# Optimization experiments

Hardware: AMD Instinct MI355X
Metric: run time of the kernel (lower is better)

## Reference

```python
import jax, jax.numpy as jnp
import numpy as np

EPS = 1e-10   # eps added inside cumprod, as in _compute_weights
FAR = 1e10    # last delta, as in forward()
NEAR_D, FAR_D = 2.0, 6.0  # typical NeRF near/far bounds for depth sampling

N_RAYS, N_PTS = 65536, 128


def setup_inputs() -> dict:
    key = jax.random.key(0)
    k1, k2, k3 = jax.random.split(key, 3)
    # densities are non-negative (raw sigma output after relu/softplus)
    density = jax.random.uniform(k1, (N_RAYS, N_PTS), dtype=jnp.float32) * 2.0
    feature = jax.random.uniform(k2, (N_RAYS, N_PTS, 3), dtype=jnp.float32)
    # monotonically increasing sample depths along each ray in [NEAR_D, FAR_D]
    depth_values = jnp.sort(
        jax.random.uniform(k3, (N_RAYS, N_PTS), dtype=jnp.float32,
                           minval=NEAR_D, maxval=FAR_D), axis=-1)
    return {"density": density, "feature": feature, "depth_values": depth_values}


def reference(density, feature, depth_values):
    # deltas: diff of sample depths, last delta = 1e10  -> [N, P]
    deltas = jnp.concatenate(
        [depth_values[..., 1:] - depth_values[..., :-1],
         jnp.full_like(depth_values[..., :1], FAR)], axis=-1)
    alpha = 1.0 - jnp.exp(-deltas * density)                      # [N, P]
    # transmittance: cumprod(1-alpha+eps) rolled right with T[...,0]=1
    Tinc = jnp.cumprod(1.0 - alpha + EPS, axis=-1)                # [N, P]
    T = jnp.concatenate([jnp.ones_like(Tinc[..., :1]), Tinc[..., :-1]], axis=-1)
    weights = T * alpha                                           # [N, P]
    # weighted feature (rgb) and depth aggregation over samples
    rgb = jnp.einsum('np,npc->nc', weights, feature)              # [N, 3]
    depth = jnp.einsum('np,npc->nc', weights,
                       jnp.broadcast_to(depth_values[..., None], feature.shape))  # [N, 3]
    return rgb, depth
```

## Files before the change

kernel.cpp:

```cpp
#include <hip/hip_runtime.h>

#define N_PTS 128
#define EPS_F 1e-10f
#define FAR_F 1e10f

template<int CTRL, int ROW_MASK>
__device__ __forceinline__ float dpp_mov(float src, float old) {
    union { float f; int i; } s, o, r;
    s.f = src; o.f = old;
    r.i = __builtin_amdgcn_update_dpp(o.i, s.i, CTRL, ROW_MASK, 0xF, false);
    return r.f;
}

__device__ __forceinline__ float wave64_reduce_add(float x) {
    x += dpp_mov<0x111, 0xF>(x, 0.0f);
    x += dpp_mov<0x112, 0xF>(x, 0.0f);
    x += dpp_mov<0x114, 0xF>(x, 0.0f);
    x += dpp_mov<0x118, 0xF>(x, 0.0f);
    x += dpp_mov<0x142, 0xA>(x, 0.0f);
    x += dpp_mov<0x143, 0xC>(x, 0.0f);
    return x;
}

__global__ __launch_bounds__(256) void volrend_kernel(
        const float* __restrict__ density,
        const float* __restrict__ feature,
        const float* __restrict__ depth,
        float* __restrict__ out, int n_rays) {
    const int lane = threadIdx.x & 63;
    const int ray  = blockIdx.x * 4 + (threadIdx.x >> 6);
    if (ray >= n_rays) return;

    const float2 dns = ((const float2*)(density + (size_t)ray * N_PTS))[lane];
    const float2 z   = ((const float2*)(depth   + (size_t)ray * N_PTS))[lane];
    const float2* fp = (const float2*)(feature + (size_t)ray * (N_PTS * 3));
    const float2 fa = fp[lane * 3 + 0];
    const float2 fb = fp[lane * 3 + 1];
    const float2 fc = fp[lane * 3 + 2];

    float nz     = dpp_mov<0x130, 0xF>(z.x, 0.0f);
    float delta0 = z.y - z.x;
    float delta1 = (lane == 63) ? FAR_F : (nz - z.y);

    float e0 = __expf(-delta0 * dns.x);
    float e1 = __expf(-delta1 * dns.y);
    float alpha0 = 1.0f - e0;
    float alpha1 = 1.0f - e1;
    float f0 = e0 + EPS_F;
    float f1 = e1 + EPS_F;

    float p = f0 * f1;
    p *= dpp_mov<0x111, 0xF>(p, 1.0f);
    p *= dpp_mov<0x112, 0xF>(p, 1.0f);
    p *= dpp_mov<0x114, 0xF>(p, 1.0f);
    p *= dpp_mov<0x118, 0xF>(p, 1.0f);
    p *= dpp_mov<0x142, 0xA>(p, 1.0f);
    p *= dpp_mov<0x143, 0xC>(p, 1.0f);
    float T0 = dpp_mov<0x138, 0xF>(p, 1.0f);

    float w0 = T0 * alpha0;
    float T1 = T0 * f0;
    float w1 = T1 * alpha1;

    float rx = wave64_reduce_add(w0 * fa.x + w1 * fb.y);
    float ry = wave64_reduce_add(w0 * fa.y + w1 * fc.x);
    float rz = wave64_reduce_add(w0 * fb.x + w1 * fc.y);
    float dd = wave64_reduce_add(w0 * z.x  + w1 * z.y);

    if (lane == 63) {
        float* o  = out + (size_t)ray * 3;
        o[0] = rx; o[1] = ry; o[2] = rz;
        float* od = out + (size_t)n_rays * 3 + (size_t)ray * 3;
        od[0] = dd; od[1] = dd; od[2] = dd;
    }
}

extern "C" void kernel_launch(void* const* d_in, const int* in_sizes, int n_in,
                              void* d_out, int out_size, void* d_ws, size_t ws_size,
                              hipStream_t stream) {
    const float* density = (const float*)d_in[0];
    const float* feature = (const float*)d_in[1];
    const float* depth   = (const float*)d_in[2];
    float* out = (float*)d_out;
    const int n_rays = in_sizes[0] / N_PTS;
    const int blocks = (n_rays + 3) / 4;
    volrend_kernel<<<blocks, 256, 0, stream>>>(density, feature, depth, out, n_rays);
}
```

Before: 188.9 us.

## Use persistent grid with half-wave per ray, float4 loads, and register prefetch

Each 64-lane wave now processes two rays, with 32 lanes per ray and four samples per lane loaded as float4. The launch becomes a persistent grid of at most 2048 blocks, each looping over ray groups and prefetching the next group's data into registers while computing the current one. Outputs are staged through double-buffered shared memory so they can be written coalesced by a few threads. The aim is wider memory transactions and hidden load latency. In exchange it adds a block-wide barrier per iteration and higher register pressure, and it assumes n_rays is a multiple of 8.

```diff
diff --git a/kernel.cpp b/kernel.cpp
--- a/kernel.cpp
+++ b/kernel.cpp
@@ -3,6 +3,8 @@
 #define N_PTS 128
 #define EPS_F 1e-10f
 #define FAR_F 1e10f
+#define RAYS_PER_BLOCK 8
+#define MAX_GRID 2048
 
 template<int CTRL, int ROW_MASK>
 __device__ __forceinline__ float dpp_mov(float src, float old) {
@@ -12,13 +14,12 @@
     return r.f;
 }
 
-__device__ __forceinline__ float wave64_reduce_add(float x) {
+__device__ __forceinline__ float half32_reduce_add(float x) {
     x += dpp_mov<0x111, 0xF>(x, 0.0f);
     x += dpp_mov<0x112, 0xF>(x, 0.0f);
     x += dpp_mov<0x114, 0xF>(x, 0.0f);
     x += dpp_mov<0x118, 0xF>(x, 0.0f);
     x += dpp_mov<0x142, 0xA>(x, 0.0f);
-    x += dpp_mov<0x143, 0xC>(x, 0.0f);
     return x;
 }
 
@@ -26,52 +27,95 @@
         const float* __restrict__ density,
         const float* __restrict__ feature,
         const float* __restrict__ depth,
-        float* __restrict__ out, int n_rays) {
+        float* __restrict__ out, int n_rays, int iters) {
     const int lane = threadIdx.x & 63;
-    const int ray  = blockIdx.x * 4 + (threadIdx.x >> 6);
-    if (ray >= n_rays) return;
+    const int sub  = lane & 31;
+    const int h    = lane >> 5;
+    const int wid  = threadIdx.x >> 6;
+    const int stride8 = gridDim.x * RAYS_PER_BLOCK;
 
-    const float2 dns = ((const float2*)(density + (size_t)ray * N_PTS))[lane];
-    const float2 z   = ((const float2*)(depth   + (size_t)ray * N_PTS))[lane];
-    const float2* fp = (const float2*)(feature + (size_t)ray * (N_PTS * 3));
-    const float2 fa = fp[lane * 3 + 0];
-    const float2 fb = fp[lane * 3 + 1];
-    const float2 fc = fp[lane * 3 + 2];
+    __shared__ float sbuf[2][64];
 
-    float nz     = dpp_mov<0x130, 0xF>(z.x, 0.0f);
-    float delta0 = z.y - z.x;
-    float delta1 = (lane == 63) ? FAR_F : (nz - z.y);
+    int base8 = blockIdx.x * RAYS_PER_BLOCK;
 
-    float e0 = __expf(-delta0 * dns.x);
-    float e1 = __expf(-delta1 * dns.y);
-    float alpha0 = 1.0f - e0;
-    float alpha1 = 1.0f - e1;
-    float f0 = e0 + EPS_F;
-    float f1 = e1 + EPS_F;
+    {
+        const int ray = base8 + (wid << 1) + h;
+        const size_t dz = (size_t)ray * N_PTS + (sub << 2);
+    }
+    int ray0 = base8 + (wid << 1) + h;
+    size_t dz0 = (size_t)ray0 * N_PTS + (sub << 2);
+    float4 dns = *(const float4*)(density + dz0);
+    float4 zz  = *(const float4*)(depth   + dz0);
+    const float4* fp0 = (const float4*)(feature + (size_t)ray0 * (N_PTS * 3) + sub * 12);
+    float4 fa = fp0[0], fb = fp0[1], fc = fp0[2];
 
-    float p = f0 * f1;
-    p *= dpp_mov<0x111, 0xF>(p, 1.0f);
-    p *= dpp_mov<0x112, 0xF>(p, 1.0f);
-    p *= dpp_mov<0x114, 0xF>(p, 1.0f);
-    p *= dpp_mov<0x118, 0xF>(p, 1.0f);
-    p *= dpp_mov<0x142, 0xA>(p, 1.0f);
-    p *= dpp_mov<0x143, 0xC>(p, 1.0f);
-    float T0 = dpp_mov<0x138, 0xF>(p, 1.0f);
+    for (int it = 0; it < iters; ++it) {
+        const bool more = (it + 1) < iters;
+        float4 ndns, nzz, nfa, nfb, nfc;
+        if (more) {
+            const int nray = base8 + stride8 + (wid << 1) + h;
+            const size_t ndz = (size_t)nray * N_PTS + (sub << 2);
+            ndns = *(const float4*)(density + ndz);
+            nzz  = *(const float4*)(depth   + ndz);
+            const float4* nfp = (const float4*)(feature + (size_t)nray * (N_PTS * 3) + sub * 12);
+            nfa = nfp[0]; nfb = nfp[1]; nfc = nfp[2];
+        }
 
-    float w0 = T0 * alpha0;
-    float T1 = T0 * f0;
-    float w1 = T1 * alpha1;
+        float nz = dpp_mov<0x130, 0xF>(zz.x, 0.0f);
+        float d0 = zz.y - zz.x;
+        float d1 = zz.z - zz.y;
+        float d2 = zz.w - zz.z;
+        float d3 = (sub == 31) ? FAR_F : (nz - zz.w);
 
-    float rx = wave64_reduce_add(w0 * fa.x + w1 * fb.y);
-    float ry = wave64_reduce_add(w0 * fa.y + w1 * fc.x);
-    float rz = wave64_reduce_add(w0 * fb.x + w1 * fc.y);
-    float dd = wave64_reduce_add(w0 * z.x  + w1 * z.y);
+        float e0 = __expf(-d0 * dns.x);
+        float e1 = __expf(-d1 * dns.y);
+        float e2 = __expf(-d2 * dns.z);
+        float e3 = __expf(-d3 * dns.w);
+        float a0 = 1.0f - e0, a1 = 1.0f - e1, a2 = 1.0f - e2, a3 = 1.0f - e3;
+        float f0 = e0 + EPS_F, f1 = e1 + EPS_F, f2 = e2 + EPS_F, f3 = e3 + EPS_F;
 
-    if (lane == 63) {
-        float* o  = out + (size_t)ray * 3;
-        o[0] = rx; o[1] = ry; o[2] = rz;
-        float* od = out + (size_t)n_rays * 3 + (size_t)ray * 3;
-        od[0] = dd; od[1] = dd; od[2] = dd;
+        float f01  = f0 * f1;
+        float f012 = f01 * f2;
+        float p    = f012 * f3;
+        p *= dpp_mov<0x111, 0xF>(p, 1.0f);
+        p *= dpp_mov<0x112, 0xF>(p, 1.0f);
+        p *= dpp_mov<0x114, 0xF>(p, 1.0f);
+        p *= dpp_mov<0x118, 0xF>(p, 1.0f);
+        p *= dpp_mov<0x142, 0xA>(p, 1.0f);
+        float Ts = dpp_mov<0x138, 0xF>(p, 1.0f);
+        if (sub == 0) Ts = 1.0f;
+
+        float w0 = Ts   * a0;
+        float T1 = Ts   * f0;   float w1 = T1 * a1;
+        float T2 = Ts   * f01;  float w2 = T2 * a2;
+        float T3 = Ts   * f012; float w3 = T3 * a3;
+
+        float rx = half32_reduce_add(w0 * fa.x + w1 * fa.w + w2 * fb.z + w3 * fc.y);
+        float ry = half32_reduce_add(w0 * fa.y + w1 * fb.x + w2 * fb.w + w3 * fc.z);
+        float rz = half32_reduce_add(w0 * fa.z + w1 * fb.y + w2 * fc.x + w3 * fc.w);
+        float dd = half32_reduce_add(w0 * zz.x + w1 * zz.y + w2 * zz.z + w3 * zz.w);
+
+        const int b = it & 1;
+        if (sub == 31) {
+            const int r8 = (wid << 1) + h;
+            sbuf[b][r8 * 3 + 0] = rx;
+            sbuf[b][r8 * 3 + 1] = ry;
+            sbuf[b][r8 * 3 + 2] = rz;
+            sbuf[b][32 + r8 * 3 + 0] = dd;
+            sbuf[b][32 + r8 * 3 + 1] = dd;
+            sbuf[b][32 + r8 * 3 + 2] = dd;
+        }
+        __syncthreads();
+        {
+            const int t = threadIdx.x;
+            float* orgb = out + (size_t)base8 * 3;
+            float* odep = out + (size_t)n_rays * 3 + (size_t)base8 * 3;
+            if (t < 24)                     orgb[t]      = sbuf[b][t];
+            else if (t >= 32 && t < 56)     odep[t - 32] = sbuf[b][t];
+        }
+
+        if (more) { dns = ndns; zz = nzz; fa = nfa; fb = nfb; fc = nfc; }
+        base8 += stride8;
     }
 }
 
@@ -83,6 +127,10 @@
     const float* depth   = (const float*)d_in[2];
     float* out = (float*)d_out;
     const int n_rays = in_sizes[0] / N_PTS;
-    const int blocks = (n_rays + 3) / 4;
-    volrend_kernel<<<blocks, 256, 0, stream>>>(density, feature, depth, out, n_rays);
+    int nblk8 = n_rays / RAYS_PER_BLOCK;
+    int grid = nblk8 < MAX_GRID ? nblk8 : MAX_GRID;
+    while (grid > 1 && (nblk8 % grid)) --grid;
+    const int iters = nblk8 / grid;
+    volrend_kernel<<<grid, 256, 0, stream>>>(density, feature, depth, out,
+                                             n_rays, iters);
 }
```

Result: slower. 193.7 us (+2.5%).
